# Optimization experiments

Measured on AMD Instinct MI355X. Metric: run time of the kernel, lower is better.

The kernel has to match this reference:

```python
import jax, jax.numpy as jnp
import numpy as np

DIM = 256
HEADS = 8
HEAD_DIM = DIM // HEADS
HIDDEN = DIM * 4


def layer_norm(x, w, b, eps=1e-5):
    m = jnp.mean(x, axis=-1, keepdims=True)
    v = jnp.mean((x - m) ** 2, axis=-1, keepdims=True)
    return (x - m) / jnp.sqrt(v + eps) * w + b


def setup_inputs() -> dict:
    key = jax.random.key(0)
    ks = jax.random.split(key, 12)
    s = lambda fan_in: 1.0 / np.sqrt(fan_in)
    inp = {
        "x0": jax.random.normal(ks[0], (2, 32, 64, DIM), jnp.float32),
        "x1": jax.random.normal(ks[1], (2, 32, 64, DIM), jnp.float32),
        # torch Linear weights stored [out, in], no bias for qk/v/merge
        "qk_w": jax.random.uniform(ks[2], (DIM, DIM), jnp.float32, -s(DIM), s(DIM)),
        "v_w": jax.random.uniform(ks[3], (DIM, DIM), jnp.float32, -s(DIM), s(DIM)),
        "merge_w": jax.random.uniform(ks[4], (DIM, DIM), jnp.float32, -s(DIM), s(DIM)),
        "ln1_w": jnp.ones((DIM,), jnp.float32),
        "ln1_b": jnp.zeros((DIM,), jnp.float32),
        "ln2_w": jnp.ones((DIM,), jnp.float32),
        "ln2_b": jnp.zeros((DIM,), jnp.float32),
        "fc1_w": jax.random.uniform(ks[5], (HIDDEN, 2 * DIM), jnp.float32, -s(2 * DIM), s(2 * DIM)),
        "fc1_b": jnp.zeros((HIDDEN,), jnp.float32),
        "fc2_w": jax.random.uniform(ks[6], (DIM, HIDDEN), jnp.float32, -s(HIDDEN), s(HIDDEN)),
        "fc2_b": jnp.zeros((DIM,), jnp.float32),
        "gamma": jnp.ones((DIM,), jnp.float32),
    }
    return inp


def reference(x0, x1, qk_w, v_w, merge_w, ln1_w, ln1_b, ln2_w, ln2_b,
              fc1_w, fc1_b, fc2_w, fc2_b, gamma):
    N0, L0, WW0, C = x0.shape
    N1, L1, WW1, _ = x1.shape
    x0f = x0.reshape(N0, L0 * WW0, C)
    x1f = x1.reshape(N1, L1 * WW1, C)

    n0 = layer_norm(x0f, ln1_w, ln1_b)
    n1 = layer_norm(x1f, ln1_w, ln1_b)

    def heads(t):  # [N, S, C] -> [N, H, S, Dh]
        N, S, _ = t.shape
        return t.reshape(N, S, HEADS, HEAD_DIM).transpose(0, 2, 1, 3)

    scale = HEAD_DIM ** -0.25  # sqrt of softmax_temp, applied to both sides
    qk0 = heads(n0 @ qk_w.T) * scale
    qk1 = heads(n1 @ qk_w.T) * scale
    v0 = heads(n0 @ v_w.T)
    v1 = heads(n1 @ v_w.T)

    # shared score matrix, reused for both softmax directions
    sim = jnp.einsum('bhld,bhsd->bhls', qk0, qk1)  # [N,H,L,S]
    attn01 = jax.nn.softmax(sim, axis=-1)
    attn10 = jax.nn.softmax(sim, axis=-2)  # == softmax(sim^T, -1)^T

    m0 = jnp.einsum('bhls,bhsd->bhld', attn01, v1)
    m1 = jnp.einsum('bhls,bhld->bhsd', attn10, v0)

    def unheads(t):  # [N,H,S,Dh] -> [N,S,C]
        N, H, S, D = t.shape
        return t.transpose(0, 2, 1, 3).reshape(N, S, H * D)

    m0 = unheads(m0) @ merge_w.T
    m1 = unheads(m1) @ merge_w.T

    def ffn_residual(x, m):
        h = jnp.concatenate([x, m], axis=-1)
        h = jax.nn.gelu(h @ fc1_w.T + fc1_b, approximate=False)
        h = h @ fc2_w.T + fc2_b
        return x + gamma * layer_norm(h, ln2_w, ln2_b)

    y0 = ffn_residual(x0f, m0).reshape(N0, L0, WW0, C)
    y1 = ffn_residual(x1f, m1).reshape(N1, L1, WW1, C)
    return (y0, y1)
```

## Files before the change

kernel.cpp:

```cpp
#include <hip/hip_runtime.h>
#include <hip/hip_bf16.h>
#include <math.h>


typedef float  f32x4  __attribute__((ext_vector_type(4)));
typedef __bf16 bf16x8 __attribute__((ext_vector_type(8)));

#define MFMA16(A, B, C) __builtin_amdgcn_mfma_f32_16x16x32_bf16((A), (B), (C), 0, 0, 0)

static constexpr int   ROWS  = 8192;
static constexpr float QK_SCALE = 0.42044820762685725f * 1.2011224087864498f;

__device__ inline unsigned short f2b(float f) {
    __hip_bfloat16 h = __float2bfloat16(f);
    union { __hip_bfloat16 h; unsigned short u; } cv;
    cv.h = h;
    return cv.u;
}

__device__ inline float exp2_fast(float x) {
#if __has_builtin(__builtin_amdgcn_exp2f)
    return __builtin_amdgcn_exp2f(x);
#else
    return __exp2f(x);
#endif
}

__device__ inline float gelu_f(float x) {
    float z = 0.7978845608028654f * (x + 0.044715f * x * x * x);
    z = fminf(fmaxf(z, -15.0f), 15.0f);
    const float e = __expf(-2.0f * z);
    const float t = (1.0f - e) / (1.0f + e);
    return 0.5f * x * (1.0f + t);
}

__global__ __launch_bounds__(256) void cvt_w_kernel(
    const float* __restrict__ qkw, const float* __restrict__ vw,
    const float* __restrict__ mw,  const float* __restrict__ w1,
    const float* __restrict__ w2,  unsigned short* __restrict__ o)
{
    int i = blockIdx.x * 256 + threadIdx.x;
    float v;
    if      (i <  65536) v = qkw[i];
    else if (i < 131072) v = vw[i - 65536];
    else if (i < 196608) v = mw[i - 131072];
    else if (i < 720896) v = w1[i - 196608];
    else                 v = w2[i - 720896];
    o[i] = f2b(v);
}

__global__ __launch_bounds__(256) void ln_in_kernel(
    const float* __restrict__ x0, const float* __restrict__ x1,
    const float* __restrict__ w,  const float* __restrict__ b,
    unsigned short* __restrict__ nb,
    unsigned short* __restrict__ acat)
{
    const int wid  = threadIdx.x >> 6;
    const int lane = threadIdx.x & 63;
    const int row  = blockIdx.x * 4 + wid;
    const float* xr = (row < 4096) ? (x0 + (size_t)row * 256)
                                   : (x1 + (size_t)(row - 4096) * 256);
    const int c0 = lane * 4;
    const float4 xv = *(const float4*)(xr + c0);
    float s  = (xv.x + xv.y) + (xv.z + xv.w);
    float sq = (xv.x * xv.x + xv.y * xv.y) + (xv.z * xv.z + xv.w * xv.w);
#pragma unroll
    for (int off = 1; off < 64; off <<= 1) {
        s  += __shfl_xor(s,  off);
        sq += __shfl_xor(sq, off);
    }
    const float mean = s * (1.0f / 256.0f);
    const float var  = sq * (1.0f / 256.0f) - mean * mean;
    const float rs   = rsqrtf(var + 1e-5f);
    const float4 wv4 = *(const float4*)(w + c0);
    const float4 bv4 = *(const float4*)(b + c0);
    ushort4 nv;
    nv.x = f2b((xv.x - mean) * rs * wv4.x + bv4.x);
    nv.y = f2b((xv.y - mean) * rs * wv4.y + bv4.y);
    nv.z = f2b((xv.z - mean) * rs * wv4.z + bv4.z);
    nv.w = f2b((xv.w - mean) * rs * wv4.w + bv4.w);
    *(ushort4*)(nb + (size_t)row * 256 + c0) = nv;
    ushort4 xb;
    xb.x = f2b(xv.x); xb.y = f2b(xv.y); xb.z = f2b(xv.z); xb.w = f2b(xv.w);
    *(ushort4*)(acat + (size_t)row * 512 + c0) = xb;
}

__global__ __launch_bounds__(256) void gemm_qkv(
    const unsigned short* __restrict__ A, const unsigned short* __restrict__ W,
    unsigned short* __restrict__ qkb, unsigned short* __restrict__ vtb)
{
    constexpr int K = 256;
    __shared__ unsigned short As[64 * 72];
    __shared__ unsigned short Ws[64 * 72];
    const int tid  = threadIdx.x;
    const int wid  = tid >> 6;
    const int lane = tid & 63;
    const int ln   = lane & 15;
    const int quad = lane >> 4;
    const int m0 = blockIdx.x * 64, n0 = blockIdx.y * 64;
    f32x4 acc[4] = {{0,0,0,0},{0,0,0,0},{0,0,0,0},{0,0,0,0}};
    const int srow = tid >> 3;
    const int skc  = (tid & 7) * 8;
    const unsigned short* aP0 = A + (size_t)(m0 + srow)      * K + skc;
    const unsigned short* aP1 = A + (size_t)(m0 + srow + 32) * K + skc;
    const unsigned short* wP0 = W + (size_t)(n0 + srow)      * K + skc;
    const unsigned short* wP1 = W + (size_t)(n0 + srow + 32) * K + skc;
    for (int k0 = 0; k0 < K; k0 += 64) {
        *(uint4*)(As + srow * 72 + skc)        = *(const uint4*)(aP0 + k0);
        *(uint4*)(As + (srow + 32) * 72 + skc) = *(const uint4*)(aP1 + k0);
        *(uint4*)(Ws + srow * 72 + skc)        = *(const uint4*)(wP0 + k0);
        *(uint4*)(Ws + (srow + 32) * 72 + skc) = *(const uint4*)(wP1 + k0);
        __syncthreads();
#pragma unroll
        for (int kk = 0; kk < 64; kk += 32) {
            const bf16x8 af = *(const bf16x8*)(As + (wid * 16 + ln) * 72 + kk + quad * 8);
#pragma unroll
            for (int f = 0; f < 4; ++f) {
                const bf16x8 wf = *(const bf16x8*)(Ws + (f * 16 + ln) * 72 + kk + quad * 8);
                acc[f] = MFMA16(wf, af, acc[f]);
            }
        }
        __syncthreads();
    }
    const int rowm = m0 + wid * 16 + ln;
    if (n0 < 256) {
#pragma unroll
        for (int f = 0; f < 4; ++f) {
            const int cb = n0 + f * 16 + quad * 4;
            ushort4 o;
            o.x = f2b(acc[f][0] * QK_SCALE); o.y = f2b(acc[f][1] * QK_SCALE);
            o.z = f2b(acc[f][2] * QK_SCALE); o.w = f2b(acc[f][3] * QK_SCALE);
            *(ushort4*)(qkb + (size_t)rowm * 256 + cb) = o;
        }
    } else {
#pragma unroll
        for (int f = 0; f < 4; ++f) {
            const int cb = (n0 - 256) + f * 16 + quad * 4;
#pragma unroll
            for (int r = 0; r < 4; ++r)
                vtb[(size_t)(cb + r) * 8192 + rowm] = f2b(acc[f][r]);
        }
    }
}

__global__ __launch_bounds__(256) void gemm_merge(
    const unsigned short* __restrict__ A, const unsigned short* __restrict__ W,
    unsigned short* __restrict__ outB)
{
    constexpr int K = 256;
    __shared__ unsigned short As[64 * 72];
    __shared__ unsigned short Ws[64 * 72];
    const int tid  = threadIdx.x;
    const int wid  = tid >> 6;
    const int lane = tid & 63;
    const int ln   = lane & 15;
    const int quad = lane >> 4;
    const int m0 = blockIdx.x * 64, n0 = blockIdx.y * 64;
    f32x4 acc[4] = {{0,0,0,0},{0,0,0,0},{0,0,0,0},{0,0,0,0}};
    const int srow = tid >> 3;
    const int skc  = (tid & 7) * 8;
    const unsigned short* aP0 = A + (size_t)(m0 + srow)      * K + skc;
    const unsigned short* aP1 = A + (size_t)(m0 + srow + 32) * K + skc;
    const unsigned short* wP0 = W + (size_t)(n0 + srow)      * K + skc;
    const unsigned short* wP1 = W + (size_t)(n0 + srow + 32) * K + skc;
    for (int k0 = 0; k0 < K; k0 += 64) {
        *(uint4*)(As + srow * 72 + skc)        = *(const uint4*)(aP0 + k0);
        *(uint4*)(As + (srow + 32) * 72 + skc) = *(const uint4*)(aP1 + k0);
        *(uint4*)(Ws + srow * 72 + skc)        = *(const uint4*)(wP0 + k0);
        *(uint4*)(Ws + (srow + 32) * 72 + skc) = *(const uint4*)(wP1 + k0);
        __syncthreads();
#pragma unroll
        for (int kk = 0; kk < 64; kk += 32) {
            const bf16x8 af = *(const bf16x8*)(As + (wid * 16 + ln) * 72 + kk + quad * 8);
#pragma unroll
            for (int f = 0; f < 4; ++f) {
                const bf16x8 wf = *(const bf16x8*)(Ws + (f * 16 + ln) * 72 + kk + quad * 8);
                acc[f] = MFMA16(wf, af, acc[f]);
            }
        }
        __syncthreads();
    }
    const int rowm = m0 + wid * 16 + ln;
#pragma unroll
    for (int f = 0; f < 4; ++f) {
        const int cb = n0 + f * 16 + quad * 4;
        ushort4 o;
        o.x = f2b(acc[f][0]); o.y = f2b(acc[f][1]);
        o.z = f2b(acc[f][2]); o.w = f2b(acc[f][3]);
        *(ushort4*)(outB + (size_t)rowm * 512 + 256 + cb) = o;
    }
}

template <bool GELU_, bool OUTB>
__global__ __launch_bounds__(256) void gemm128(
    const unsigned short* __restrict__ A, const unsigned short* __restrict__ W,
    const float* __restrict__ bias,
    unsigned short* __restrict__ outB, float* __restrict__ outF,
    int K, int NS)
{
    __shared__ unsigned short As[128 * 72];
    __shared__ unsigned short Ws[128 * 72];
    const int tid  = threadIdx.x;
    const int wid  = tid >> 6;
    const int lane = tid & 63;
    const int ln   = lane & 15;
    const int quad = lane >> 4;
    const int m0 = blockIdx.x * 128, n0 = blockIdx.y * 128;
    const int wm = (wid & 1) * 64, wn = (wid >> 1) * 64;
    f32x4 acc[4][4];
#pragma unroll
    for (int f = 0; f < 4; ++f)
#pragma unroll
        for (int i = 0; i < 4; ++i) acc[f][i] = (f32x4){0, 0, 0, 0};
    const int sr = tid >> 2;
    const int sc = (tid & 3) * 8;
    for (int k0 = 0; k0 < K; k0 += 64) {
        const unsigned short* aB = A + (size_t)m0 * K + k0;
        const unsigned short* wB = W + (size_t)n0 * K + k0;
        *(uint4*)(As + sr * 72 + sc)             = *(const uint4*)(aB + (size_t)sr * K + sc);
        *(uint4*)(As + sr * 72 + sc + 32)        = *(const uint4*)(aB + (size_t)sr * K + sc + 32);
        *(uint4*)(As + (sr + 64) * 72 + sc)      = *(const uint4*)(aB + (size_t)(sr + 64) * K + sc);
        *(uint4*)(As + (sr + 64) * 72 + sc + 32) = *(const uint4*)(aB + (size_t)(sr + 64) * K + sc + 32);
        *(uint4*)(Ws + sr * 72 + sc)             = *(const uint4*)(wB + (size_t)sr * K + sc);
        *(uint4*)(Ws + sr * 72 + sc + 32)        = *(const uint4*)(wB + (size_t)sr * K + sc + 32);
        *(uint4*)(Ws + (sr + 64) * 72 + sc)      = *(const uint4*)(wB + (size_t)(sr + 64) * K + sc);
        *(uint4*)(Ws + (sr + 64) * 72 + sc + 32) = *(const uint4*)(wB + (size_t)(sr + 64) * K + sc + 32);
        __syncthreads();
#pragma unroll
        for (int kk = 0; kk < 64; kk += 32) {
            bf16x8 af[4], wf[4];
#pragma unroll
            for (int i = 0; i < 4; ++i)
                af[i] = *(const bf16x8*)(As + (wm + i * 16 + ln) * 72 + kk + quad * 8);
#pragma unroll
            for (int f = 0; f < 4; ++f)
                wf[f] = *(const bf16x8*)(Ws + (wn + f * 16 + ln) * 72 + kk + quad * 8);
#pragma unroll
            for (int f = 0; f < 4; ++f)
#pragma unroll
                for (int i = 0; i < 4; ++i)
                    acc[f][i] = MFMA16(wf[f], af[i], acc[f][i]);
        }
        __syncthreads();
    }
#pragma unroll
    for (int f = 0; f < 4; ++f) {
        const int feat = n0 + wn + f * 16 + quad * 4;
        const float4 b4 = *(const float4*)(bias + feat);
#pragma unroll
        for (int i = 0; i < 4; ++i) {
            const int token = m0 + wm + i * 16 + ln;
            float vv[4] = {acc[f][i][0] + b4.x, acc[f][i][1] + b4.y,
                           acc[f][i][2] + b4.z, acc[f][i][3] + b4.w};
            if (GELU_) {
#pragma unroll
                for (int r = 0; r < 4; ++r) vv[r] = gelu_f(vv[r]);
            }
            if (OUTB) {
                ushort4 o;
                o.x = f2b(vv[0]); o.y = f2b(vv[1]); o.z = f2b(vv[2]); o.w = f2b(vv[3]);
                *(ushort4*)(outB + (size_t)token * NS + feat) = o;
            } else {
                float4 o = {vv[0], vv[1], vv[2], vv[3]};
                *(float4*)(outF + (size_t)token * NS + feat) = o;
            }
        }
    }
}

__global__ __launch_bounds__(256, 4) void attn_kernel(
    const unsigned short* __restrict__ qk, const unsigned short* __restrict__ vtb,
    unsigned short* __restrict__ mo)
{
    __shared__ unsigned short Pw[4][64 * 32];
    const int tid  = threadIdx.x;
    const int wid  = tid >> 6;
    const int lane = tid & 63;
    const int ln   = lane & 15;
    const int quad = lane >> 4;
    const int dir = blockIdx.z, bh = blockIdx.y;
    const int b = bh >> 3, h = bh & 7;
    const int qbase = b * 2048 + (dir ? 4096 : 0);
    const int kbase = b * 2048 + (dir ? 0 : 4096);
    const int q0 = blockIdx.x * 64;
    const int xsw = ((ln >> 1) & 1) << 4;

    bf16x8 qf[4];
#pragma unroll
    for (int qg = 0; qg < 4; ++qg)
        qf[qg] = *(const bf16x8*)(qk + (size_t)(qbase + q0 + qg * 16 + ln) * 256 + h * 32 + quad * 8);

    f32x4 oacc[4][2];
#pragma unroll
    for (int qg = 0; qg < 4; ++qg) {
        oacc[qg][0] = (f32x4){0, 0, 0, 0};
        oacc[qg][1] = (f32x4){0, 0, 0, 0};
    }
    float lp[4] = {0.0f, 0.0f, 0.0f, 0.0f};
    const f32x4 zf = {0, 0, 0, 0};

    const unsigned short* kp = qk  + (size_t)(kbase + wid * 32 + ln) * 256 + h * 32 + quad * 8;
    const unsigned short* vp = vtb + (size_t)(h * 32 + ln) * 8192 + (kbase + wid * 32) + quad * 8;

    unsigned short* Pq[4];
#pragma unroll
    for (int qg = 0; qg < 4; ++qg) Pq[qg] = &Pw[wid][(qg * 16 + ln) * 32];

    bf16x8 kc0 = *(const bf16x8*)(kp);
    bf16x8 kc1 = *(const bf16x8*)(kp + 16 * 256);
    bf16x8 vc0 = *(const bf16x8*)(vp);
    bf16x8 vc1 = *(const bf16x8*)(vp + 16 * 8192);
    bf16x8 vn0, vn1;

    for (int it = 0; it < 16; ++it) {
#pragma unroll
        for (int sub = 0; sub < 2; ++sub) {
            const bf16x8 kf = sub ? kc1 : kc0;
            f32x4 s[4];
#pragma unroll
            for (int qg = 0; qg < 4; ++qg) s[qg] = MFMA16(kf, qf[qg], zf);
#pragma unroll
            for (int qg = 0; qg < 4; ++qg) {
                const float e0 = exp2_fast(s[qg][0]), e1 = exp2_fast(s[qg][1]);
                const float e2 = exp2_fast(s[qg][2]), e3 = exp2_fast(s[qg][3]);
                lp[qg] += (e0 + e1) + (e2 + e3);
                ushort4 pb;
                pb.x = f2b(e0); pb.y = f2b(e1); pb.z = f2b(e2); pb.w = f2b(e3);
                *(ushort4*)(Pq[qg] + ((sub * 16 + quad * 4) ^ xsw)) = pb;
            }
        }
        if (it < 15) {
            const unsigned short* kn = kp + (size_t)(it + 1) * 128 * 256;
            const unsigned short* vn = vp + (it + 1) * 128;
            kc0 = *(const bf16x8*)(kn);
            kc1 = *(const bf16x8*)(kn + 16 * 256);
            vn0 = *(const bf16x8*)(vn);
            vn1 = *(const bf16x8*)(vn + 16 * 8192);
        }
        asm volatile("s_waitcnt lgkmcnt(0)" ::: "memory");
#pragma unroll
        for (int qg = 0; qg < 4; ++qg) {
            const bf16x8 pf = *(const bf16x8*)(Pq[qg] + ((quad * 8) ^ xsw));
            oacc[qg][0] = MFMA16(vc0, pf, oacc[qg][0]);
            oacc[qg][1] = MFMA16(vc1, pf, oacc[qg][1]);
        }
        if (it < 15) { vc0 = vn0; vc1 = vn1; }
    }

#pragma unroll
    for (int qg = 0; qg < 4; ++qg) {
        lp[qg] += __shfl_xor(lp[qg], 16);
        lp[qg] += __shfl_xor(lp[qg], 32);
    }
    __syncthreads();
    float* scr  = (float*)&Pw[0][0];
    float* Lbuf = scr;
    float* Obuf = scr + 256;
    if (quad == 0) {
#pragma unroll
        for (int qg = 0; qg < 4; ++qg) Lbuf[wid * 64 + qg * 16 + ln] = lp[qg];
    }
#pragma unroll
    for (int qg = 0; qg < 4; ++qg) {
#pragma unroll
        for (int dg = 0; dg < 2; ++dg)
            *(f32x4*)&Obuf[(wid * 2 + dg) * 256 + lane * 4] = oacc[qg][dg];
        __syncthreads();
        if (wid == qg) {
            const int q = qg * 16 + ln;
            const float rinv = 1.0f /
                (Lbuf[q] + Lbuf[64 + q] + Lbuf[128 + q] + Lbuf[192 + q]);
            const size_t orow = (size_t)(qbase + q0 + q) * 256 + h * 32;
#pragma unroll
            for (int dg = 0; dg < 2; ++dg) {
                f32x4 sum = *(f32x4*)&Obuf[(0 + dg) * 256 + lane * 4];
#pragma unroll
                for (int w = 1; w < 4; ++w)
                    sum += *(f32x4*)&Obuf[(w * 2 + dg) * 256 + lane * 4];
                ushort4 o;
                o.x = f2b(sum[0] * rinv); o.y = f2b(sum[1] * rinv);
                o.z = f2b(sum[2] * rinv); o.w = f2b(sum[3] * rinv);
                *(ushort4*)(mo + orow + dg * 16 + quad * 4) = o;
            }
        }
        __syncthreads();
    }
}

__global__ __launch_bounds__(256) void ln_out_kernel(
    const float* __restrict__ x0, const float* __restrict__ x1,
    const float* __restrict__ h2, const float* __restrict__ w,
    const float* __restrict__ b,  const float* __restrict__ gamma,
    float* __restrict__ out)
{
    const int wid  = threadIdx.x >> 6;
    const int lane = threadIdx.x & 63;
    const int row  = blockIdx.x * 4 + wid;
    const int c0 = lane * 4;
    const float4 hv = *(const float4*)(h2 + (size_t)row * 256 + c0);
    float s  = (hv.x + hv.y) + (hv.z + hv.w);
    float sq = (hv.x * hv.x + hv.y * hv.y) + (hv.z * hv.z + hv.w * hv.w);
#pragma unroll
    for (int off = 1; off < 64; off <<= 1) {
        s  += __shfl_xor(s,  off);
        sq += __shfl_xor(sq, off);
    }
    const float mean = s * (1.0f / 256.0f);
    const float var  = sq * (1.0f / 256.0f) - mean * mean;
    const float rs   = rsqrtf(var + 1e-5f);
    const float* xr = (row < 4096) ? (x0 + (size_t)row * 256)
                                   : (x1 + (size_t)(row - 4096) * 256);
    const float4 xv = *(const float4*)(xr + c0);
    const float4 w4 = *(const float4*)(w + c0);
    const float4 b4 = *(const float4*)(b + c0);
    const float4 g4 = *(const float4*)(gamma + c0);
    float4 y;
    y.x = xv.x + g4.x * ((hv.x - mean) * rs * w4.x + b4.x);
    y.y = xv.y + g4.y * ((hv.y - mean) * rs * w4.y + b4.y);
    y.z = xv.z + g4.z * ((hv.z - mean) * rs * w4.z + b4.z);
    y.w = xv.w + g4.w * ((hv.w - mean) * rs * w4.w + b4.w);
    *(float4*)(out + (size_t)row * 256 + c0) = y;
}

extern "C" void kernel_launch(void* const* d_in, const int* in_sizes, int n_in,
                              void* d_out, int out_size, void* d_ws, size_t ws_size,
                              hipStream_t stream) {
    (void)in_sizes; (void)n_in; (void)out_size; (void)ws_size;
    const float* x0      = (const float*)d_in[0];
    const float* x1      = (const float*)d_in[1];
    const float* qk_w    = (const float*)d_in[2];
    const float* v_w     = (const float*)d_in[3];
    const float* merge_w = (const float*)d_in[4];
    const float* ln1_w   = (const float*)d_in[5];
    const float* ln1_b   = (const float*)d_in[6];
    const float* ln2_w   = (const float*)d_in[7];
    const float* ln2_b   = (const float*)d_in[8];
    const float* fc1_w   = (const float*)d_in[9];
    const float* fc1_b   = (const float*)d_in[10];
    const float* fc2_w   = (const float*)d_in[11];
    const float* fc2_b   = (const float*)d_in[12];
    const float* gamma   = (const float*)d_in[13];
    float* out = (float*)d_out;

    unsigned short* nb   = (unsigned short*)d_ws;
    unsigned short* qkb  = nb   + (size_t)ROWS * 256;
    unsigned short* vtb  = qkb  + (size_t)ROWS * 256;
    unsigned short* mb   = vtb  + (size_t)ROWS * 256;
    unsigned short* acat = mb   + (size_t)ROWS * 256;
    unsigned short* fc1o = acat + (size_t)ROWS * 512;
    float*          h2   = (float*)(fc1o + (size_t)ROWS * 1024);
    unsigned short* wqv  = (unsigned short*)(h2 + (size_t)ROWS * 256);
    unsigned short* wm   = wqv + 131072;
    unsigned short* w1   = wm  + 65536;
    unsigned short* w2   = w1  + 524288;

    cvt_w_kernel<<<3840, 256, 0, stream>>>(qk_w, v_w, merge_w, fc1_w, fc2_w, wqv);
    ln_in_kernel<<<2048, 256, 0, stream>>>(x0, x1, ln1_w, ln1_b, nb, acat);

    gemm_qkv<<<dim3(128, 8), 256, 0, stream>>>(nb, wqv, qkb, vtb);

    attn_kernel<<<dim3(32, 16, 2), 256, 0, stream>>>(qkb, vtb, mb);

    gemm_merge<<<dim3(128, 4), 256, 0, stream>>>(mb, wm, acat);

    gemm128<true, true><<<dim3(64, 8), 256, 0, stream>>>(
        acat, w1, fc1_b, fc1o, nullptr, 512, 1024);
    gemm128<false, false><<<dim3(64, 2), 256, 0, stream>>>(
        fc1o, w2, fc2_b, nullptr, h2, 1024, 256);

    ln_out_kernel<<<2048, 256, 0, stream>>>(x0, x1, h2, ln2_w, ln2_b, gamma, out);
}
```

Before: 183.5 us.

## Feed softmax probabilities directly from registers into 16x16x16 MFMA for PV

Removes the LDS round-trip for the probability tile in the attention kernel. The exp'd scores in the QK^T MFMA output layout are packed straight into bf16x4 operands of the 16x16x16 bf16 MFMA, and V is loaded as matching 4-element fragments. This drops the LDS stores and loads and the lgkmcnt wait, at the cost of twice as many smaller MFMAs. K/V prefetch also moves to the top of the loop for better latency hiding, and the shared buffer is shrunk to the epilogue scratch.

```diff
diff --git a/kernel.cpp b/kernel.cpp
--- a/kernel.cpp
+++ b/kernel.cpp
@@ -5,8 +5,10 @@
 
 typedef float  f32x4  __attribute__((ext_vector_type(4)));
 typedef __bf16 bf16x8 __attribute__((ext_vector_type(8)));
-
-#define MFMA16(A, B, C) __builtin_amdgcn_mfma_f32_16x16x32_bf16((A), (B), (C), 0, 0, 0)
+typedef short  s16x4  __attribute__((ext_vector_type(4)));
+
+#define MFMA16(A, B, C)  __builtin_amdgcn_mfma_f32_16x16x32_bf16((A), (B), (C), 0, 0, 0)
+#define MFMAK16(A, B, C) __builtin_amdgcn_mfma_f32_16x16x16bf16_1k((A), (B), (C), 0, 0, 0)
 
 static constexpr int   ROWS  = 8192;
 static constexpr float QK_SCALE = 0.42044820762685725f * 1.2011224087864498f;
@@ -272,7 +274,7 @@
     const unsigned short* __restrict__ qk, const unsigned short* __restrict__ vtb,
     unsigned short* __restrict__ mo)
 {
-    __shared__ unsigned short Pw[4][64 * 32];
+    __shared__ float scr[2304];
     const int tid  = threadIdx.x;
     const int wid  = tid >> 6;
     const int lane = tid & 63;
@@ -283,7 +285,6 @@
     const int qbase = b * 2048 + (dir ? 4096 : 0);
     const int kbase = b * 2048 + (dir ? 0 : 4096);
     const int q0 = blockIdx.x * 64;
-    const int xsw = ((ln >> 1) & 1) << 4;
 
     bf16x8 qf[4];
 #pragma unroll
@@ -300,19 +301,30 @@
     const f32x4 zf = {0, 0, 0, 0};
 
     const unsigned short* kp = qk  + (size_t)(kbase + wid * 32 + ln) * 256 + h * 32 + quad * 8;
-    const unsigned short* vp = vtb + (size_t)(h * 32 + ln) * 8192 + (kbase + wid * 32) + quad * 8;
-
-    unsigned short* Pq[4];
-#pragma unroll
-    for (int qg = 0; qg < 4; ++qg) Pq[qg] = &Pw[wid][(qg * 16 + ln) * 32];
+    const unsigned short* vp = vtb + (size_t)(h * 32 + ln) * 8192 + (kbase + wid * 32) + quad * 4;
 
     bf16x8 kc0 = *(const bf16x8*)(kp);
     bf16x8 kc1 = *(const bf16x8*)(kp + 16 * 256);
-    bf16x8 vc0 = *(const bf16x8*)(vp);
-    bf16x8 vc1 = *(const bf16x8*)(vp + 16 * 8192);
-    bf16x8 vn0, vn1;
+    s16x4 vc[2][2], vn[2][2];
+#pragma unroll
+    for (int s = 0; s < 2; ++s)
+#pragma unroll
+        for (int dg = 0; dg < 2; ++dg)
+            vc[s][dg] = *(const s16x4*)(vp + s * 16 + dg * 16 * 8192);
+    bf16x8 kn0, kn1;
 
     for (int it = 0; it < 16; ++it) {
+        if (it < 15) {
+            const unsigned short* kpn = kp + (size_t)(it + 1) * 128 * 256;
+            const unsigned short* vpn = vp + (it + 1) * 128;
+            kn0 = *(const bf16x8*)(kpn);
+            kn1 = *(const bf16x8*)(kpn + 16 * 256);
+#pragma unroll
+            for (int s = 0; s < 2; ++s)
+#pragma unroll
+                for (int dg = 0; dg < 2; ++dg)
+                    vn[s][dg] = *(const s16x4*)(vpn + s * 16 + dg * 16 * 8192);
+        }
 #pragma unroll
         for (int sub = 0; sub < 2; ++sub) {
             const bf16x8 kf = sub ? kc1 : kc0;
@@ -324,27 +336,21 @@
                 const float e0 = exp2_fast(s[qg][0]), e1 = exp2_fast(s[qg][1]);
                 const float e2 = exp2_fast(s[qg][2]), e3 = exp2_fast(s[qg][3]);
                 lp[qg] += (e0 + e1) + (e2 + e3);
-                ushort4 pb;
-                pb.x = f2b(e0); pb.y = f2b(e1); pb.z = f2b(e2); pb.w = f2b(e3);
-                *(ushort4*)(Pq[qg] + ((sub * 16 + quad * 4) ^ xsw)) = pb;
+                s16x4 p;
+                p[0] = (short)f2b(e0); p[1] = (short)f2b(e1);
+                p[2] = (short)f2b(e2); p[3] = (short)f2b(e3);
+                oacc[qg][0] = MFMAK16(vc[sub][0], p, oacc[qg][0]);
+                oacc[qg][1] = MFMAK16(vc[sub][1], p, oacc[qg][1]);
             }
         }
         if (it < 15) {
-            const unsigned short* kn = kp + (size_t)(it + 1) * 128 * 256;
-            const unsigned short* vn = vp + (it + 1) * 128;
-            kc0 = *(const bf16x8*)(kn);
-            kc1 = *(const bf16x8*)(kn + 16 * 256);
-            vn0 = *(const bf16x8*)(vn);
-            vn1 = *(const bf16x8*)(vn + 16 * 8192);
-        }
-        asm volatile("s_waitcnt lgkmcnt(0)" ::: "memory");
-#pragma unroll
-        for (int qg = 0; qg < 4; ++qg) {
-            const bf16x8 pf = *(const bf16x8*)(Pq[qg] + ((quad * 8) ^ xsw));
-            oacc[qg][0] = MFMA16(vc0, pf, oacc[qg][0]);
-            oacc[qg][1] = MFMA16(vc1, pf, oacc[qg][1]);
-        }
-        if (it < 15) { vc0 = vn0; vc1 = vn1; }
+            kc0 = kn0; kc1 = kn1;
+#pragma unroll
+            for (int s = 0; s < 2; ++s)
+#pragma unroll
+                for (int dg = 0; dg < 2; ++dg)
+                    vc[s][dg] = vn[s][dg];
+        }
     }
 
 #pragma unroll
@@ -353,7 +359,6 @@
         lp[qg] += __shfl_xor(lp[qg], 32);
     }
     __syncthreads();
-    float* scr  = (float*)&Pw[0][0];
     float* Lbuf = scr;
     float* Obuf = scr + 256;
     if (quad == 0) {
```

Result: slower. 197.6 us (+7.7%).
